# Kernel tuning notes

Measured on AMD Instinct MI355X. Metric: run time of the kernel, lower is better.

The kernel has to match this reference:

```python
import jax, jax.numpy as jnp
import numpy as np

N, E, D, H, ED = 50000, 600000, 128, 2, 5
C = D // H  # per-head channels = 64


def _lin(k, fan_in, fan_out):
    return jax.random.normal(k, (fan_out, fan_in), jnp.float32) / np.sqrt(fan_in)


def setup_inputs() -> dict:
    key = jax.random.key(0)
    ks = jax.random.split(key, 12)
    return {
        "x": jax.random.normal(ks[0], (N, D), jnp.float32),
        "edge_index": jax.random.randint(ks[1], (2, E), 0, N, dtype=jnp.int32),
        "edge_attr": jax.random.normal(ks[2], (E, ED), jnp.float32),
        "Wq": _lin(ks[3], D, D), "bq": jnp.zeros((D,), jnp.float32),
        "Wk": _lin(ks[4], D, D), "bk": jnp.zeros((D,), jnp.float32),
        "Wv": _lin(ks[5], D, D), "bv": jnp.zeros((D,), jnp.float32),
        "We": _lin(ks[6], ED, D),                       # lin_edge, bias=False in PyG
        "Wskip": _lin(ks[7], D, D), "bskip": jnp.zeros((D,), jnp.float32),
        "Wbeta": _lin(ks[8], 3 * D, 1),                 # lin_beta, bias=False
        "Wproj": _lin(ks[9], D, D), "bproj": jnp.zeros((D,), jnp.float32),
    }


def reference(x, edge_index, edge_attr, Wq, bq, Wk, bk, Wv, bv, We,
              Wskip, bskip, Wbeta, Wproj, bproj):
    src, dst = edge_index[0], edge_index[1]
    # node projections -> [N, H, C]
    q = (x @ Wq.T + bq).reshape(N, H, C)
    k = (x @ Wk.T + bk).reshape(N, H, C)
    v = (x @ Wv.T + bv).reshape(N, H, C)
    e = (edge_attr @ We.T).reshape(E, H, C)
    # gather per-edge, fold in edge features
    kj = k[src] + e                                   # [E, H, C]
    vj = v[src] + e                                   # [E, H, C]
    alpha = (q[dst] * kj).sum(-1) / np.sqrt(C)        # [E, H]
    # segment softmax over edges grouped by dst node
    amax = jax.ops.segment_max(alpha, dst, num_segments=N)   # [N, H]
    ex = jnp.exp(alpha - amax[dst])
    denom = jax.ops.segment_sum(ex, dst, num_segments=N)     # [N, H]
    w = ex / denom[dst]                               # [E, H]
    # scatter-aggregate weighted values, concat heads
    out = jax.ops.segment_sum(vj * w[:, :, None], dst, num_segments=N).reshape(N, D)
    # beta-gated skip connection
    x_r = x @ Wskip.T + bskip
    beta = jax.nn.sigmoid(jnp.concatenate([out, x_r, out - x_r], axis=-1) @ Wbeta.T)  # [N,1]
    out = beta * x_r + (1.0 - beta) * out
    # outer projection (dropout is identity in eval)
    return out @ Wproj.T + bproj
```

## Files before the change

kernel.cpp:

```cpp
#include <hip/hip_runtime.h>
#include <stdint.h>
#include <math.h>

#define D 128
#define EDIM 5

typedef __attribute__((ext_vector_type(8))) short bf16x8;
typedef __attribute__((ext_vector_type(4))) float f32x4;

__device__ __forceinline__ ushort f2b(float f) {
  union { float f; uint u; } v; v.f = f;
  uint u = v.u;
  return (ushort)((u + 0x7fff + ((u >> 16) & 1)) >> 16);
}
__device__ __forceinline__ float blo(uint u) {
  union { uint u; float f; } v; v.u = u << 16; return v.f;
}
__device__ __forceinline__ float bhi(uint u) {
  union { uint u; float f; } v; v.u = u & 0xffff0000u; return v.f;
}


__global__ void zero_int_kernel(int* __restrict__ p, int n) {
  int i = blockIdx.x * blockDim.x + threadIdx.x;
  if (i < n) p[i] = 0;
}

__global__ void hist_kernel(const int* __restrict__ ei, int* __restrict__ deg, int E) {
  int e = blockIdx.x * blockDim.x + threadIdx.x;
  if (e < E) atomicAdd(&deg[ei[(size_t)E + e]], 1);
}

__global__ __launch_bounds__(256) void scan_p1(const int* __restrict__ deg,
                                               int* __restrict__ off,
                                               int* __restrict__ blockSum, int n4) {
  __shared__ int waveTot[4];
  int idx = blockIdx.x * 256 + threadIdx.x;
  int4 v = make_int4(0, 0, 0, 0);
  if (idx < n4) v = ((const int4*)deg)[idx];
  int c0 = v.x, c1 = c0 + v.y, c2 = c1 + v.z, c3 = c2 + v.w;
  int tot = c3;
  int lane = threadIdx.x & 63, w = threadIdx.x >> 6;
  int incl = tot;
#pragma unroll
  for (int ofs = 1; ofs < 64; ofs <<= 1) {
    int t = __shfl_up(incl, ofs, 64);
    if (lane >= ofs) incl += t;
  }
  if (lane == 63) waveTot[w] = incl;
  __syncthreads();
  int wbase = 0;
  for (int i = 0; i < w; ++i) wbase += waveTot[i];
  int excl = wbase + incl - tot;
  if (idx < n4) {
    int4 o;
    o.x = excl; o.y = excl + c0; o.z = excl + c1; o.w = excl + c2;
    ((int4*)off)[idx] = o;
  }
  if (threadIdx.x == 255) blockSum[blockIdx.x] = wbase + incl;
}

__global__ void scan_p2(const int* __restrict__ blockSum, int* __restrict__ blockBase,
                        int* __restrict__ off_last, int nb) {
  int lane = threadIdx.x;
  int v = (lane < nb) ? blockSum[lane] : 0;
  int incl = v;
#pragma unroll
  for (int ofs = 1; ofs < 64; ofs <<= 1) {
    int t = __shfl_up(incl, ofs, 64);
    if (lane >= ofs) incl += t;
  }
  if (lane < nb) blockBase[lane] = incl - v;
  if (lane == 63) *off_last = incl;
}

__global__ __launch_bounds__(256) void scan_p3(int* __restrict__ off,
                                               const int* __restrict__ blockBase, int n4) {
  int idx = blockIdx.x * 256 + threadIdx.x;
  if (idx >= n4) return;
  int b = blockBase[blockIdx.x];
  int4 v = ((int4*)off)[idx];
  v.x += b; v.y += b; v.z += b; v.w += b;
  ((int4*)off)[idx] = v;
}

__global__ void scatter_kernel(const int* __restrict__ ei, const float* __restrict__ ea,
                               const int* __restrict__ off, int* __restrict__ cursor,
                               int* __restrict__ ssrc, uint4* __restrict__ easrt, int E) {
  int e = blockIdx.x * blockDim.x + threadIdx.x;
  if (e >= E) return;
  int dst = ei[(size_t)E + e];
  int pos = off[dst] + atomicAdd(&cursor[dst], 1);
  ssrc[pos] = ei[e];
  const float* p = ea + (size_t)e * EDIM;
  uint e0 = f2b(p[0]), e1 = f2b(p[1]), e2 = f2b(p[2]), e3 = f2b(p[3]), e4 = f2b(p[4]);
  easrt[pos] = make_uint4(e0 | (e1 << 16), e2 | (e3 << 16), e4, 0);
}


__global__ void cvt_x_kernel(const float* __restrict__ x, ushort* __restrict__ xb, int n4) {
  int i = blockIdx.x * blockDim.x + threadIdx.x;
  if (i >= n4) return;
  float4 v = ((const float4*)x)[i];
  ushort4 o;
  o.x = f2b(v.x); o.y = f2b(v.y); o.z = f2b(v.z); o.w = f2b(v.w);
  ((ushort4*)xb)[i] = o;
}

__global__ void cvt_w_kernel(const float* __restrict__ Wq, const float* __restrict__ Wk,
                             const float* __restrict__ Wv, const float* __restrict__ Wr,
                             const float* __restrict__ bq, const float* __restrict__ bk,
                             const float* __restrict__ bv, const float* __restrict__ br,
                             const float* __restrict__ Wp,
                             ushort* __restrict__ Wcat, float* __restrict__ bcat,
                             ushort* __restrict__ Wpb) {
  int i = blockIdx.x * blockDim.x + threadIdx.x;
  if (i < 512 * D) {
    int r = i >> 7;
    float v;
    if (r < 128)      v = Wq[i] * 0.125f;
    else if (r < 256) v = Wk[i - 128 * D];
    else if (r < 384) v = Wv[i - 256 * D];
    else              v = Wr[i - 384 * D];
    Wcat[i] = f2b(v);
  }
  if (i < D * D) Wpb[i] = f2b(Wp[i]);
  if (i < 512) {
    float v = (i < 128) ? bq[i] * 0.125f
            : (i < 256) ? bk[i - 128]
            : (i < 384) ? bv[i - 256] : br[i - 384];
    bcat[i] = v;
  }
}

template <int MODE>
__global__ __launch_bounds__(256) void gemm_kernel(
    const ushort* __restrict__ A, const ushort* __restrict__ B,
    const float* __restrict__ bias,
    float* __restrict__ q, ushort* __restrict__ kv, float* __restrict__ xr,
    float* __restrict__ out, int M)
{
  __shared__ __attribute__((aligned(16))) ushort As[128][128];
  __shared__ __attribute__((aligned(16))) ushort Bs[128][128];
  const int tid = threadIdx.x;
  const int rowBase = blockIdx.x * 128;
  const int colBase = blockIdx.y * 128;

#pragma unroll
  for (int it = 0; it < 8; ++it) {
    int i = it * 256 + tid;
    int r = i >> 4, c = i & 15;
    int sw = (c ^ (r & 7)) * 8;
    int gr = rowBase + r;
    uint4 av = make_uint4(0, 0, 0, 0);
    if (gr < M) av = *(const uint4*)(A + (size_t)gr * D + c * 8);
    *(uint4*)(&As[r][sw]) = av;
    uint4 bv4 = *(const uint4*)(B + (size_t)(colBase + r) * D + c * 8);
    *(uint4*)(&Bs[r][sw]) = bv4;
  }
  __syncthreads();

  const int lane = tid & 63;
  const int wave = tid >> 6;
  const int wm = (wave >> 1) * 64;
  const int wn = (wave & 1) * 64;
  const int lrow = lane & 15;
  const int kgrp = lane >> 4;

  f32x4 acc[4][4] = {};
#pragma unroll
  for (int ks = 0; ks < 4; ++ks) {
    int chunk = ks * 4 + kgrp;
    bf16x8 a[4], b[4];
#pragma unroll
    for (int m = 0; m < 4; ++m) {
      int r = wm + m * 16 + lrow;
      a[m] = *(const bf16x8*)&As[r][(chunk ^ (r & 7)) * 8];
    }
#pragma unroll
    for (int n = 0; n < 4; ++n) {
      int r = wn + n * 16 + lrow;
      b[n] = *(const bf16x8*)&Bs[r][(chunk ^ (r & 7)) * 8];
    }
#pragma unroll
    for (int m = 0; m < 4; ++m)
#pragma unroll
      for (int n = 0; n < 4; ++n)
        acc[m][n] = __builtin_amdgcn_mfma_f32_16x16x32_bf16(a[m], b[n], acc[m][n], 0, 0, 0);
  }

  const int orow = (lane >> 4) * 4;
  const int ocol = lane & 15;
#pragma unroll
  for (int m = 0; m < 4; ++m) {
#pragma unroll
    for (int n = 0; n < 4; ++n) {
      int col = colBase + wn + n * 16 + ocol;
      float bi = bias[col];
#pragma unroll
      for (int i = 0; i < 4; ++i) {
        int gr = rowBase + wm + m * 16 + orow + i;
        if (gr >= M) continue;
        float v = acc[m][n][i] + bi;
        if (MODE == 0) {
          int sel = col >> 7, c = col & 127;
          if (sel == 0)      q[(size_t)gr * D + c] = v;
          else if (sel == 1) kv[(size_t)gr * 2 * D + c] = f2b(v);
          else if (sel == 2) kv[(size_t)gr * 2 * D + D + c] = f2b(v);
          else               xr[(size_t)gr * D + c] = v;
        } else {
          out[(size_t)gr * D + col] = v;
        }
      }
    }
  }
}

__global__ __launch_bounds__(256) void node_attn_kernel(
    const float* __restrict__ q, const ushort* __restrict__ kv,
    const float* __restrict__ xr, ushort* __restrict__ g,
    const uint4* __restrict__ easrt, const float* __restrict__ We,
    const float* __restrict__ Wb,
    const int* __restrict__ off, const int* __restrict__ ssrc, int N)
{
  const int wid = threadIdx.x >> 6;
  const int lane = threadIdx.x & 63;
  const int node = blockIdx.x * 4 + wid;
  if (node >= N) return;
  const int grp = lane >> 4;
  const int i = lane & 15;
  const int di = i * 8;

  float qr[8];
  {
    float4 a = *(const float4*)(q + (size_t)node * D + di);
    float4 b = *(const float4*)(q + (size_t)node * D + di + 4);
    qr[0] = a.x; qr[1] = a.y; qr[2] = a.z; qr[3] = a.w;
    qr[4] = b.x; qr[5] = b.y; qr[6] = b.z; qr[7] = b.w;
  }

  float qwe[5];
  {
    const float* wp = We + (size_t)di * EDIM;
    float4 w[10];
#pragma unroll
    for (int t = 0; t < 10; ++t) w[t] = *(const float4*)(wp + 4 * t);
#pragma unroll
    for (int j = 0; j < 5; ++j) {
      float s = 0.f;
#pragma unroll
      for (int r = 0; r < 8; ++r) {
        int idx = r * 5 + j;
        s += qr[r] * ((const float*)&w[idx >> 2])[idx & 3];
      }
      qwe[j] = s;
    }
#pragma unroll
    for (int ofs = 1; ofs < 8; ofs <<= 1)
#pragma unroll
      for (int j = 0; j < 5; ++j) qwe[j] += __shfl_xor(qwe[j], ofs, 64);
  }

  const int beg = off[node], end = off[node + 1];
  float m = -INFINITY, s = 0.f;
  float o[8] = {0.f, 0.f, 0.f, 0.f, 0.f, 0.f, 0.f, 0.f};
  float wea[5] = {0.f, 0.f, 0.f, 0.f, 0.f};

  for (int pb = beg; pb < end; pb += 4) {
    int p = pb + grp;
    bool valid = p < end;
    int pl = valid ? p : beg;
    int src = ssrc[pl];
    uint4 eau = easrt[pl];
    float ea0 = blo(eau.x), ea1 = bhi(eau.x);
    float ea2 = blo(eau.y), ea3 = bhi(eau.y);
    float ea4 = blo(eau.z);

    const ushort* kp = kv + (size_t)src * 2 * D;
    uint4 ku = *(const uint4*)(kp + di);
    uint4 vu = *(const uint4*)(kp + D + di);

    float part = qr[0] * blo(ku.x) + qr[1] * bhi(ku.x)
               + qr[2] * blo(ku.y) + qr[3] * bhi(ku.y)
               + qr[4] * blo(ku.z) + qr[5] * bhi(ku.z)
               + qr[6] * blo(ku.w) + qr[7] * bhi(ku.w);
#pragma unroll
    for (int ofs = 1; ofs < 8; ofs <<= 1) part += __shfl_xor(part, ofs, 64);
    float eadot = qwe[0] * ea0 + qwe[1] * ea1 + qwe[2] * ea2 + qwe[3] * ea3 + qwe[4] * ea4;
    float alpha = valid ? (part + eadot) : -INFINITY;

    float nm = fmaxf(m, alpha);
    float scale = (m > -1e30f) ? __expf(m - nm) : 0.f;
    float pw = (alpha > -1e30f) ? __expf(alpha - nm) : 0.f;
    m = nm;
    s = s * scale + pw;
    o[0] = o[0] * scale + pw * blo(vu.x);
    o[1] = o[1] * scale + pw * bhi(vu.x);
    o[2] = o[2] * scale + pw * blo(vu.y);
    o[3] = o[3] * scale + pw * bhi(vu.y);
    o[4] = o[4] * scale + pw * blo(vu.z);
    o[5] = o[5] * scale + pw * bhi(vu.z);
    o[6] = o[6] * scale + pw * blo(vu.w);
    o[7] = o[7] * scale + pw * bhi(vu.w);
    wea[0] = wea[0] * scale + pw * ea0;
    wea[1] = wea[1] * scale + pw * ea1;
    wea[2] = wea[2] * scale + pw * ea2;
    wea[3] = wea[3] * scale + pw * ea3;
    wea[4] = wea[4] * scale + pw * ea4;
  }

#pragma unroll
  for (int ofs = 16; ofs < 64; ofs <<= 1) {
    float m2 = __shfl_xor(m, ofs, 64);
    float s2 = __shfl_xor(s, ofs, 64);
    float o2[8], w2[5];
#pragma unroll
    for (int j = 0; j < 8; ++j) o2[j] = __shfl_xor(o[j], ofs, 64);
#pragma unroll
    for (int j = 0; j < 5; ++j) w2[j] = __shfl_xor(wea[j], ofs, 64);
    float nm = fmaxf(m, m2);
    float e1 = (m > -1e30f) ? __expf(m - nm) : 0.f;
    float e2 = (m2 > -1e30f) ? __expf(m2 - nm) : 0.f;
    s = s * e1 + s2 * e2;
#pragma unroll
    for (int j = 0; j < 8; ++j) o[j] = o[j] * e1 + o2[j] * e2;
#pragma unroll
    for (int j = 0; j < 5; ++j) wea[j] = wea[j] * e1 + w2[j] * e2;
    m = nm;
  }

  float inv = (s > 0.f) ? (1.f / s) : 0.f;
#pragma unroll
  for (int j = 0; j < 8; ++j) o[j] *= inv;
#pragma unroll
  for (int j = 0; j < 5; ++j) wea[j] *= inv;

  {
    const float* wp = We + (size_t)di * EDIM;
    float4 w[10];
#pragma unroll
    for (int t = 0; t < 10; ++t) w[t] = *(const float4*)(wp + 4 * t);
#pragma unroll
    for (int r = 0; r < 8; ++r)
#pragma unroll
      for (int j = 0; j < 5; ++j) {
        int idx = r * 5 + j;
        o[r] += wea[j] * ((const float*)&w[idx >> 2])[idx & 3];
      }
  }

  float xrv[8];
  {
    float4 a = *(const float4*)(xr + (size_t)node * D + di);
    float4 b = *(const float4*)(xr + (size_t)node * D + di + 4);
    xrv[0] = a.x; xrv[1] = a.y; xrv[2] = a.z; xrv[3] = a.w;
    xrv[4] = b.x; xrv[5] = b.y; xrv[6] = b.z; xrv[7] = b.w;
  }
  float part = 0.f;
#pragma unroll
  for (int r = 0; r < 8; ++r) {
    float w1 = Wb[di + r] + Wb[256 + di + r];
    float w2 = Wb[128 + di + r] - Wb[256 + di + r];
    part += o[r] * w1 + xrv[r] * w2;
  }
#pragma unroll
  for (int ofs = 1; ofs < 16; ofs <<= 1) part += __shfl_xor(part, ofs, 64);
  float beta = 1.f / (1.f + __expf(-part));

  if (grp == 0) {
    uint pk[4];
#pragma unroll
    for (int r = 0; r < 4; ++r) {
      float g0 = beta * xrv[2 * r] + (1.f - beta) * o[2 * r];
      float g1 = beta * xrv[2 * r + 1] + (1.f - beta) * o[2 * r + 1];
      pk[r] = (uint)f2b(g0) | ((uint)f2b(g1) << 16);
    }
    *(uint4*)(g + (size_t)node * D + di) = make_uint4(pk[0], pk[1], pk[2], pk[3]);
  }
}


extern "C" void kernel_launch(void* const* d_in, const int* in_sizes, int n_in,
                              void* d_out, int out_size, void* d_ws, size_t ws_size,
                              hipStream_t stream)
{
  const float* x  = (const float*)d_in[0];
  const int*   ei = (const int*)d_in[1];
  const float* ea = (const float*)d_in[2];
  const float* Wq = (const float*)d_in[3];
  const float* bq = (const float*)d_in[4];
  const float* Wk = (const float*)d_in[5];
  const float* bk = (const float*)d_in[6];
  const float* Wv = (const float*)d_in[7];
  const float* bv = (const float*)d_in[8];
  const float* We = (const float*)d_in[9];
  const float* Wr = (const float*)d_in[10];
  const float* br = (const float*)d_in[11];
  const float* Wb = (const float*)d_in[12];
  const float* Wp = (const float*)d_in[13];
  const float* bp = (const float*)d_in[14];

  const int N = in_sizes[0] / D;
  const int E = in_sizes[1] / 2;
  float* out = (float*)d_out;

  char* ws = (char*)d_ws;
  size_t o = 0;
  auto alloc = [&](size_t bytes) -> void* {
    void* p = ws + o;
    o = (o + bytes + 255) & ~(size_t)255;
    return p;
  };
  ushort* xb     = (ushort*)alloc((size_t)N * D * sizeof(ushort));
  float*  q      = (float*)alloc((size_t)N * D * sizeof(float));
  ushort* kv     = (ushort*)alloc((size_t)N * 2 * D * sizeof(ushort));
  float*  xr     = (float*)alloc((size_t)N * D * sizeof(float));
  ushort* g      = (ushort*)alloc((size_t)N * D * sizeof(ushort));
  ushort* Wcat   = (ushort*)alloc((size_t)512 * D * sizeof(ushort));
  float*  bcat   = (float*)alloc(512 * sizeof(float));
  ushort* Wpb    = (ushort*)alloc((size_t)D * D * sizeof(ushort));
  int*    deg    = (int*)alloc((size_t)N * sizeof(int));
  int*    cursor = (int*)alloc((size_t)N * sizeof(int));
  int*    offs   = (int*)alloc((size_t)(N + 1) * sizeof(int));
  int*    ssrc   = (int*)alloc((size_t)E * sizeof(int));
  uint4*  easrt  = (uint4*)alloc((size_t)E * sizeof(uint4));
  int*    bsum   = (int*)alloc(64 * sizeof(int));
  int*    bbase  = (int*)alloc(64 * sizeof(int));

  const int n4 = N / 4;
  const int nb = (n4 + 255) / 256;

  zero_int_kernel<<<(N + 255) / 256, 256, 0, stream>>>(deg, N);
  zero_int_kernel<<<(N + 255) / 256, 256, 0, stream>>>(cursor, N);
  hist_kernel<<<(E + 255) / 256, 256, 0, stream>>>(ei, deg, E);
  scan_p1<<<nb, 256, 0, stream>>>(deg, offs, bsum, n4);
  scan_p2<<<1, 64, 0, stream>>>(bsum, bbase, offs + N, nb);
  scan_p3<<<nb, 256, 0, stream>>>(offs, bbase, n4);
  scatter_kernel<<<(E + 255) / 256, 256, 0, stream>>>(ei, ea, offs, cursor, ssrc, easrt, E);

  cvt_x_kernel<<<(N * D / 4 + 255) / 256, 256, 0, stream>>>(x, xb, N * D / 4);
  cvt_w_kernel<<<(512 * D + 255) / 256, 256, 0, stream>>>(Wq, Wk, Wv, Wr, bq, bk, bv, br,
                                                          Wp, Wcat, bcat, Wpb);

  dim3 g0((N + 127) / 128, 4);
  gemm_kernel<0><<<g0, 256, 0, stream>>>(xb, Wcat, bcat, q, kv, xr, nullptr, N);

  node_attn_kernel<<<(N + 3) / 4, 256, 0, stream>>>(q, kv, xr, g, easrt, We, Wb,
                                                    offs, ssrc, N);

  dim3 g1((N + 127) / 128, 1);
  gemm_kernel<1><<<g1, 256, 0, stream>>>(g, Wpb, bp, nullptr, nullptr, nullptr, out, N);
}
```

Before: 256.0 us.

## Fuse x conversion into projection GEMM, precompute q·We, lazy softmax rescale

Removes the separate x-to-bf16 and cursor-zeroing kernels by folding them into the projection GEMM and scan kernels. Adds a folded Wq·We block to the weight matrix so the GEMM also emits per-node q·We terms, replacing the per-node shuffle reduction in the attention kernel. Stores q and x_r as bf16 instead of fp32 to cut memory traffic, and uses 64-row GEMM tiles that loop over all five column blocks. The attention loop now prefetches the next edge's gather and skips the online-softmax rescale unless the running max grows by more than a threshold. These trade some precision and a larger GEMM per block for fewer launches and less traffic.

Result: faster. 241.2 us (-5.8%).

```diff
diff --git a/kernel.cpp b/kernel.cpp
--- a/kernel.cpp
+++ b/kernel.cpp
@@ -75,13 +75,15 @@
 }
 
 __global__ __launch_bounds__(256) void scan_p3(int* __restrict__ off,
-                                               const int* __restrict__ blockBase, int n4) {
+                                               const int* __restrict__ blockBase,
+                                               int* __restrict__ cursor, int n4) {
   int idx = blockIdx.x * 256 + threadIdx.x;
   if (idx >= n4) return;
   int b = blockBase[blockIdx.x];
   int4 v = ((int4*)off)[idx];
   v.x += b; v.y += b; v.z += b; v.w += b;
   ((int4*)off)[idx] = v;
+  ((int4*)cursor)[idx] = make_int4(0, 0, 0, 0);
 }
 
 __global__ void scatter_kernel(const int* __restrict__ ei, const float* __restrict__ ea,
@@ -97,21 +99,11 @@
   easrt[pos] = make_uint4(e0 | (e1 << 16), e2 | (e3 << 16), e4, 0);
 }
 
-
-__global__ void cvt_x_kernel(const float* __restrict__ x, ushort* __restrict__ xb, int n4) {
-  int i = blockIdx.x * blockDim.x + threadIdx.x;
-  if (i >= n4) return;
-  float4 v = ((const float4*)x)[i];
-  ushort4 o;
-  o.x = f2b(v.x); o.y = f2b(v.y); o.z = f2b(v.z); o.w = f2b(v.w);
-  ((ushort4*)xb)[i] = o;
-}
-
 __global__ void cvt_w_kernel(const float* __restrict__ Wq, const float* __restrict__ Wk,
                              const float* __restrict__ Wv, const float* __restrict__ Wr,
                              const float* __restrict__ bq, const float* __restrict__ bk,
                              const float* __restrict__ bv, const float* __restrict__ br,
-                             const float* __restrict__ Wp,
+                             const float* __restrict__ We, const float* __restrict__ Wp,
                              ushort* __restrict__ Wcat, float* __restrict__ bcat,
                              ushort* __restrict__ Wpb) {
   int i = blockIdx.x * blockDim.x + threadIdx.x;
@@ -123,6 +115,18 @@
     else if (r < 384) v = Wv[i - 256 * D];
     else              v = Wr[i - 384 * D];
     Wcat[i] = f2b(v);
+  } else if (i < 512 * D + 128 * D) {
+    int ie = i - 512 * D;
+    int r = ie >> 7, c = ie & 127;
+    int h = r >> 3, j = r & 7;
+    float v = 0.f;
+    if (h < 2 && j < 5) {
+      for (int d = 0; d < 64; ++d) {
+        int dd = h * 64 + d;
+        v += We[(size_t)dd * EDIM + j] * 0.125f * Wq[(size_t)dd * D + c];
+      }
+    }
+    Wcat[(size_t)(512 + r) * D + c] = f2b(v);
   }
   if (i < D * D) Wpb[i] = f2b(Wp[i]);
   if (i < 512) {
@@ -130,50 +134,155 @@
             : (i < 256) ? bk[i - 128]
             : (i < 384) ? bv[i - 256] : br[i - 384];
     bcat[i] = v;
-  }
-}
-
-template <int MODE>
-__global__ __launch_bounds__(256) void gemm_kernel(
-    const ushort* __restrict__ A, const ushort* __restrict__ B,
-    const float* __restrict__ bias,
-    float* __restrict__ q, ushort* __restrict__ kv, float* __restrict__ xr,
-    float* __restrict__ out, int M)
+  } else if (i < 640) {
+    int t = i - 512;
+    int h = t >> 3, j = t & 7;
+    float v = 0.f;
+    if (h < 2 && j < 5) {
+      for (int d = 0; d < 64; ++d) {
+        int dd = h * 64 + d;
+        v += bq[dd] * 0.125f * We[(size_t)dd * EDIM + j];
+      }
+    }
+    bcat[i] = v;
+  }
+}
+
+__global__ __launch_bounds__(256) void proj_gemm_kernel(
+    const float* __restrict__ x, const ushort* __restrict__ Wcat,
+    const float* __restrict__ bcat,
+    ushort* __restrict__ q, ushort* __restrict__ kv, ushort* __restrict__ xr,
+    float* __restrict__ qwe, int M)
 {
-  __shared__ __attribute__((aligned(16))) ushort As[128][128];
+  __shared__ __attribute__((aligned(16))) ushort As[64][128];
   __shared__ __attribute__((aligned(16))) ushort Bs[128][128];
   const int tid = threadIdx.x;
-  const int rowBase = blockIdx.x * 128;
-  const int colBase = blockIdx.y * 128;
-
+  const int rowBase = blockIdx.x * 64;
+
+#pragma unroll
+  for (int it = 0; it < 4; ++it) {
+    int i = it * 256 + tid;
+    int r = i >> 4, c = i & 15;
+    int gr = rowBase + r;
+    float4 a0 = make_float4(0.f, 0.f, 0.f, 0.f), a1 = a0;
+    if (gr < M) {
+      a0 = *(const float4*)(x + (size_t)gr * D + c * 8);
+      a1 = *(const float4*)(x + (size_t)gr * D + c * 8 + 4);
+    }
+    uint4 w;
+    w.x = (uint)f2b(a0.x) | ((uint)f2b(a0.y) << 16);
+    w.y = (uint)f2b(a0.z) | ((uint)f2b(a0.w) << 16);
+    w.z = (uint)f2b(a1.x) | ((uint)f2b(a1.y) << 16);
+    w.w = (uint)f2b(a1.z) | ((uint)f2b(a1.w) << 16);
+    *(uint4*)(&As[r][(c ^ (r & 7)) * 8]) = w;
+  }
+
+  const int lane = tid & 63;
+  const int wave = tid >> 6;
+  const int wm = (wave >> 1) * 32;
+  const int wn = (wave & 1) * 64;
+  const int lrow = lane & 15;
+  const int kgrp = lane >> 4;
+  const int orow = (lane >> 4) * 4;
+  const int ocol = lane & 15;
+
+  for (int cb = 0; cb < 5; ++cb) {
+#pragma unroll
+    for (int it = 0; it < 8; ++it) {
+      int i = it * 256 + tid;
+      int r = i >> 4, c = i & 15;
+      uint4 bv4 = *(const uint4*)(Wcat + (size_t)(cb * 128 + r) * D + c * 8);
+      *(uint4*)(&Bs[r][(c ^ (r & 7)) * 8]) = bv4;
+    }
+    __syncthreads();
+
+    f32x4 acc[2][4] = {};
+#pragma unroll
+    for (int ks = 0; ks < 4; ++ks) {
+      int chunk = ks * 4 + kgrp;
+      bf16x8 a[2], b[4];
+#pragma unroll
+      for (int m = 0; m < 2; ++m) {
+        int r = wm + m * 16 + lrow;
+        a[m] = *(const bf16x8*)&As[r][(chunk ^ (r & 7)) * 8];
+      }
+#pragma unroll
+      for (int n = 0; n < 4; ++n) {
+        int r = wn + n * 16 + lrow;
+        b[n] = *(const bf16x8*)&Bs[r][(chunk ^ (r & 7)) * 8];
+      }
+#pragma unroll
+      for (int m = 0; m < 2; ++m)
+#pragma unroll
+        for (int n = 0; n < 4; ++n)
+          acc[m][n] = __builtin_amdgcn_mfma_f32_16x16x32_bf16(a[m], b[n], acc[m][n], 0, 0, 0);
+    }
+
+#pragma unroll
+    for (int m = 0; m < 2; ++m) {
+#pragma unroll
+      for (int n = 0; n < 4; ++n) {
+        int col = cb * 128 + wn + n * 16 + ocol;
+        float bi = bcat[col];
+        int sel = col >> 7, c = col & 127;
+#pragma unroll
+        for (int ii = 0; ii < 4; ++ii) {
+          int gr = rowBase + wm + m * 16 + orow + ii;
+          if (gr >= M) continue;
+          float v = acc[m][n][ii] + bi;
+          if (sel == 0)      q[(size_t)gr * D + c] = f2b(v);
+          else if (sel == 1) kv[(size_t)gr * 2 * D + c] = f2b(v);
+          else if (sel == 2) kv[(size_t)gr * 2 * D + D + c] = f2b(v);
+          else if (sel == 3) xr[(size_t)gr * D + c] = f2b(v);
+          else if (c < 16)   qwe[(size_t)gr * 16 + c] = v;
+        }
+      }
+    }
+    __syncthreads();
+  }
+}
+
+__global__ __launch_bounds__(256) void out_gemm_kernel(
+    const ushort* __restrict__ g, const ushort* __restrict__ Wpb,
+    const float* __restrict__ bp, float* __restrict__ out, int M)
+{
+  __shared__ __attribute__((aligned(16))) ushort As[64][128];
+  __shared__ __attribute__((aligned(16))) ushort Bs[128][128];
+  const int tid = threadIdx.x;
+  const int rowBase = blockIdx.x * 64;
+
+#pragma unroll
+  for (int it = 0; it < 4; ++it) {
+    int i = it * 256 + tid;
+    int r = i >> 4, c = i & 15;
+    int gr = rowBase + r;
+    uint4 av = make_uint4(0, 0, 0, 0);
+    if (gr < M) av = *(const uint4*)(g + (size_t)gr * D + c * 8);
+    *(uint4*)(&As[r][(c ^ (r & 7)) * 8]) = av;
+  }
 #pragma unroll
   for (int it = 0; it < 8; ++it) {
     int i = it * 256 + tid;
     int r = i >> 4, c = i & 15;
-    int sw = (c ^ (r & 7)) * 8;
-    int gr = rowBase + r;
-    uint4 av = make_uint4(0, 0, 0, 0);
-    if (gr < M) av = *(const uint4*)(A + (size_t)gr * D + c * 8);
-    *(uint4*)(&As[r][sw]) = av;
-    uint4 bv4 = *(const uint4*)(B + (size_t)(colBase + r) * D + c * 8);
-    *(uint4*)(&Bs[r][sw]) = bv4;
+    uint4 bv4 = *(const uint4*)(Wpb + (size_t)r * D + c * 8);
+    *(uint4*)(&Bs[r][(c ^ (r & 7)) * 8]) = bv4;
   }
   __syncthreads();
 
   const int lane = tid & 63;
   const int wave = tid >> 6;
-  const int wm = (wave >> 1) * 64;
+  const int wm = (wave >> 1) * 32;
   const int wn = (wave & 1) * 64;
   const int lrow = lane & 15;
   const int kgrp = lane >> 4;
 
-  f32x4 acc[4][4] = {};
+  f32x4 acc[2][4] = {};
 #pragma unroll
   for (int ks = 0; ks < 4; ++ks) {
     int chunk = ks * 4 + kgrp;
-    bf16x8 a[4], b[4];
-#pragma unroll
-    for (int m = 0; m < 4; ++m) {
+    bf16x8 a[2], b[4];
+#pragma unroll
+    for (int m = 0; m < 2; ++m) {
       int r = wm + m * 16 + lrow;
       a[m] = *(const bf16x8*)&As[r][(chunk ^ (r & 7)) * 8];
     }
@@ -183,7 +292,7 @@
       b[n] = *(const bf16x8*)&Bs[r][(chunk ^ (r & 7)) * 8];
     }
 #pragma unroll
-    for (int m = 0; m < 4; ++m)
+    for (int m = 0; m < 2; ++m)
 #pragma unroll
       for (int n = 0; n < 4; ++n)
         acc[m][n] = __builtin_amdgcn_mfma_f32_16x16x32_bf16(a[m], b[n], acc[m][n], 0, 0, 0);
@@ -192,35 +301,26 @@
   const int orow = (lane >> 4) * 4;
   const int ocol = lane & 15;
 #pragma unroll
-  for (int m = 0; m < 4; ++m) {
+  for (int m = 0; m < 2; ++m) {
 #pragma unroll
     for (int n = 0; n < 4; ++n) {
-      int col = colBase + wn + n * 16 + ocol;
-      float bi = bias[col];
-#pragma unroll
-      for (int i = 0; i < 4; ++i) {
-        int gr = rowBase + wm + m * 16 + orow + i;
+      int col = wn + n * 16 + ocol;
+      float bi = bp[col];
+#pragma unroll
+      for (int ii = 0; ii < 4; ++ii) {
+        int gr = rowBase + wm + m * 16 + orow + ii;
         if (gr >= M) continue;
-        float v = acc[m][n][i] + bi;
-        if (MODE == 0) {
-          int sel = col >> 7, c = col & 127;
-          if (sel == 0)      q[(size_t)gr * D + c] = v;
-          else if (sel == 1) kv[(size_t)gr * 2 * D + c] = f2b(v);
-          else if (sel == 2) kv[(size_t)gr * 2 * D + D + c] = f2b(v);
-          else               xr[(size_t)gr * D + c] = v;
-        } else {
-          out[(size_t)gr * D + col] = v;
-        }
+        out[(size_t)gr * D + col] = acc[m][n][ii] + bi;
       }
     }
   }
 }
 
 __global__ __launch_bounds__(256) void node_attn_kernel(
-    const float* __restrict__ q, const ushort* __restrict__ kv,
-    const float* __restrict__ xr, ushort* __restrict__ g,
-    const uint4* __restrict__ easrt, const float* __restrict__ We,
-    const float* __restrict__ Wb,
+    const ushort* __restrict__ q, const ushort* __restrict__ kv,
+    const ushort* __restrict__ xr, ushort* __restrict__ g,
+    const float* __restrict__ qwe, const uint4* __restrict__ easrt,
+    const float* __restrict__ We, const float* __restrict__ Wb,
     const int* __restrict__ off, const int* __restrict__ ssrc, int N)
 {
   const int wid = threadIdx.x >> 6;
@@ -230,35 +330,19 @@
   const int grp = lane >> 4;
   const int i = lane & 15;
   const int di = i * 8;
+  const int head = i >> 3;
 
   float qr[8];
   {
-    float4 a = *(const float4*)(q + (size_t)node * D + di);
-    float4 b = *(const float4*)(q + (size_t)node * D + di + 4);
-    qr[0] = a.x; qr[1] = a.y; qr[2] = a.z; qr[3] = a.w;
-    qr[4] = b.x; qr[5] = b.y; qr[6] = b.z; qr[7] = b.w;
-  }
-
-  float qwe[5];
+    uint4 qa = *(const uint4*)(q + (size_t)node * D + di);
+    qr[0] = blo(qa.x); qr[1] = bhi(qa.x); qr[2] = blo(qa.y); qr[3] = bhi(qa.y);
+    qr[4] = blo(qa.z); qr[5] = bhi(qa.z); qr[6] = blo(qa.w); qr[7] = bhi(qa.w);
+  }
+  float qw[5];
   {
-    const float* wp = We + (size_t)di * EDIM;
-    float4 w[10];
-#pragma unroll
-    for (int t = 0; t < 10; ++t) w[t] = *(const float4*)(wp + 4 * t);
-#pragma unroll
-    for (int j = 0; j < 5; ++j) {
-      float s = 0.f;
-#pragma unroll
-      for (int r = 0; r < 8; ++r) {
-        int idx = r * 5 + j;
-        s += qr[r] * ((const float*)&w[idx >> 2])[idx & 3];
-      }
-      qwe[j] = s;
-    }
-#pragma unroll
-    for (int ofs = 1; ofs < 8; ofs <<= 1)
-#pragma unroll
-      for (int j = 0; j < 5; ++j) qwe[j] += __shfl_xor(qwe[j], ofs, 64);
+    const float* qp = qwe + (size_t)node * 16 + head * 8;
+    float4 t = *(const float4*)qp;
+    qw[0] = t.x; qw[1] = t.y; qw[2] = t.z; qw[3] = t.w; qw[4] = qp[4];
   }
 
   const int beg = off[node], end = off[node + 1];
@@ -266,47 +350,65 @@
   float o[8] = {0.f, 0.f, 0.f, 0.f, 0.f, 0.f, 0.f, 0.f};
   float wea[5] = {0.f, 0.f, 0.f, 0.f, 0.f};
 
-  for (int pb = beg; pb < end; pb += 4) {
-    int p = pb + grp;
-    bool valid = p < end;
-    int pl = valid ? p : beg;
-    int src = ssrc[pl];
-    uint4 eau = easrt[pl];
-    float ea0 = blo(eau.x), ea1 = bhi(eau.x);
-    float ea2 = blo(eau.y), ea3 = bhi(eau.y);
-    float ea4 = blo(eau.z);
-
-    const ushort* kp = kv + (size_t)src * 2 * D;
-    uint4 ku = *(const uint4*)(kp + di);
-    uint4 vu = *(const uint4*)(kp + D + di);
-
-    float part = qr[0] * blo(ku.x) + qr[1] * bhi(ku.x)
-               + qr[2] * blo(ku.y) + qr[3] * bhi(ku.y)
-               + qr[4] * blo(ku.z) + qr[5] * bhi(ku.z)
-               + qr[6] * blo(ku.w) + qr[7] * bhi(ku.w);
-#pragma unroll
-    for (int ofs = 1; ofs < 8; ofs <<= 1) part += __shfl_xor(part, ofs, 64);
-    float eadot = qwe[0] * ea0 + qwe[1] * ea1 + qwe[2] * ea2 + qwe[3] * ea3 + qwe[4] * ea4;
-    float alpha = valid ? (part + eadot) : -INFINITY;
-
-    float nm = fmaxf(m, alpha);
-    float scale = (m > -1e30f) ? __expf(m - nm) : 0.f;
-    float pw = (alpha > -1e30f) ? __expf(alpha - nm) : 0.f;
-    m = nm;
-    s = s * scale + pw;
-    o[0] = o[0] * scale + pw * blo(vu.x);
-    o[1] = o[1] * scale + pw * bhi(vu.x);
-    o[2] = o[2] * scale + pw * blo(vu.y);
-    o[3] = o[3] * scale + pw * bhi(vu.y);
-    o[4] = o[4] * scale + pw * blo(vu.z);
-    o[5] = o[5] * scale + pw * bhi(vu.z);
-    o[6] = o[6] * scale + pw * blo(vu.w);
-    o[7] = o[7] * scale + pw * bhi(vu.w);
-    wea[0] = wea[0] * scale + pw * ea0;
-    wea[1] = wea[1] * scale + pw * ea1;
-    wea[2] = wea[2] * scale + pw * ea2;
-    wea[3] = wea[3] * scale + pw * ea3;
-    wea[4] = wea[4] * scale + pw * ea4;
+  if (beg < end) {
+    int p0 = beg + grp;
+    bool valid_c = p0 < end;
+    int pl = valid_c ? p0 : beg;
+    int src_c = ssrc[pl];
+    uint4 eau_c = easrt[pl];
+    const ushort* kp0 = kv + (size_t)src_c * (2 * D);
+    uint4 ku_c = *(const uint4*)(kp0 + di);
+    uint4 vu_c = *(const uint4*)(kp0 + D + di);
+
+    for (int pb = beg; pb < end; pb += 4) {
+      int pn = pb + 4 + grp;
+      bool valid_n = pn < end;
+      int pln = valid_n ? pn : pl;
+      int src_n = ssrc[pln];
+      uint4 eau_n = easrt[pln];
+
+      float ea0 = blo(eau_c.x), ea1 = bhi(eau_c.x), ea2 = blo(eau_c.y),
+            ea3 = bhi(eau_c.y), ea4 = blo(eau_c.z);
+      float part = qr[0] * blo(ku_c.x) + qr[1] * bhi(ku_c.x)
+                 + qr[2] * blo(ku_c.y) + qr[3] * bhi(ku_c.y)
+                 + qr[4] * blo(ku_c.z) + qr[5] * bhi(ku_c.z)
+                 + qr[6] * blo(ku_c.w) + qr[7] * bhi(ku_c.w);
+#pragma unroll
+      for (int ofs = 1; ofs < 8; ofs <<= 1) part += __shfl_xor(part, ofs, 64);
+      float eadot = qw[0] * ea0 + qw[1] * ea1 + qw[2] * ea2 + qw[3] * ea3 + qw[4] * ea4;
+      float alpha = valid_c ? (part + eadot) : -INFINITY;
+
+      const ushort* kpn = kv + (size_t)src_n * (2 * D);
+      uint4 ku_n = *(const uint4*)(kpn + di);
+      uint4 vu_n = *(const uint4*)(kpn + D + di);
+
+      float v0 = blo(vu_c.x), v1 = bhi(vu_c.x), v2 = blo(vu_c.y), v3 = bhi(vu_c.y),
+            v4 = blo(vu_c.z), v5 = bhi(vu_c.z), v6 = blo(vu_c.w), v7 = bhi(vu_c.w);
+
+      if (__any(alpha > m + 8.f)) {
+        float nm = fmaxf(m, alpha);
+        float scale = (m > -1e30f) ? __expf(m - nm) : 0.f;
+        float pw = (alpha > -1e30f) ? __expf(alpha - nm) : 0.f;
+        m = nm;
+        s = s * scale + pw;
+        o[0] = o[0] * scale + pw * v0; o[1] = o[1] * scale + pw * v1;
+        o[2] = o[2] * scale + pw * v2; o[3] = o[3] * scale + pw * v3;
+        o[4] = o[4] * scale + pw * v4; o[5] = o[5] * scale + pw * v5;
+        o[6] = o[6] * scale + pw * v6; o[7] = o[7] * scale + pw * v7;
+        wea[0] = wea[0] * scale + pw * ea0; wea[1] = wea[1] * scale + pw * ea1;
+        wea[2] = wea[2] * scale + pw * ea2; wea[3] = wea[3] * scale + pw * ea3;
+        wea[4] = wea[4] * scale + pw * ea4;
+      } else {
+        float pw = (alpha > -1e30f) ? __expf(alpha - m) : 0.f;
+        s += pw;
+        o[0] += pw * v0; o[1] += pw * v1; o[2] += pw * v2; o[3] += pw * v3;
+        o[4] += pw * v4; o[5] += pw * v5; o[6] += pw * v6; o[7] += pw * v7;
+        wea[0] += pw * ea0; wea[1] += pw * ea1; wea[2] += pw * ea2;
+        wea[3] += pw * ea3; wea[4] += pw * ea4;
+      }
+
+      ku_c = ku_n; vu_c = vu_n; eau_c = eau_n; valid_c = valid_n; pl = pln;
+    }
   }
 
 #pragma unroll
@@ -351,10 +453,9 @@
 
   float xrv[8];
   {
-    float4 a = *(const float4*)(xr + (size_t)node * D + di);
-    float4 b = *(const float4*)(xr + (size_t)node * D + di + 4);
-    xrv[0] = a.x; xrv[1] = a.y; xrv[2] = a.z; xrv[3] = a.w;
-    xrv[4] = b.x; xrv[5] = b.y; xrv[6] = b.z; xrv[7] = b.w;
+    uint4 xa = *(const uint4*)(xr + (size_t)node * D + di);
+    xrv[0] = blo(xa.x); xrv[1] = bhi(xa.x); xrv[2] = blo(xa.y); xrv[3] = bhi(xa.y);
+    xrv[4] = blo(xa.z); xrv[5] = bhi(xa.z); xrv[6] = blo(xa.w); xrv[7] = bhi(xa.w);
   }
   float part = 0.f;
 #pragma unroll
@@ -411,13 +512,13 @@
     o = (o + bytes + 255) & ~(size_t)255;
     return p;
   };
-  ushort* xb     = (ushort*)alloc((size_t)N * D * sizeof(ushort));
-  float*  q      = (float*)alloc((size_t)N * D * sizeof(float));
+  ushort* q      = (ushort*)alloc((size_t)N * D * sizeof(ushort));
   ushort* kv     = (ushort*)alloc((size_t)N * 2 * D * sizeof(ushort));
-  float*  xr     = (float*)alloc((size_t)N * D * sizeof(float));
+  ushort* xr     = (ushort*)alloc((size_t)N * D * sizeof(ushort));
   ushort* g      = (ushort*)alloc((size_t)N * D * sizeof(ushort));
-  ushort* Wcat   = (ushort*)alloc((size_t)512 * D * sizeof(ushort));
-  float*  bcat   = (float*)alloc(512 * sizeof(float));
+  float*  qwe    = (float*)alloc((size_t)N * 16 * sizeof(float));
+  ushort* Wcat   = (ushort*)alloc((size_t)640 * D * sizeof(ushort));
+  float*  bcat   = (float*)alloc(640 * sizeof(float));
   ushort* Wpb    = (ushort*)alloc((size_t)D * D * sizeof(ushort));
   int*    deg    = (int*)alloc((size_t)N * sizeof(int));
   int*    cursor = (int*)alloc((size_t)N * sizeof(int));
@@ -431,23 +532,19 @@
   const int nb = (n4 + 255) / 256;
 
   zero_int_kernel<<<(N + 255) / 256, 256, 0, stream>>>(deg, N);
-  zero_int_kernel<<<(N + 255) / 256, 256, 0, stream>>>(cursor, N);
   hist_kernel<<<(E + 255) / 256, 256, 0, stream>>>(ei, deg, E);
   scan_p1<<<nb, 256, 0, stream>>>(deg, offs, bsum, n4);
   scan_p2<<<1, 64, 0, stream>>>(bsum, bbase, offs + N, nb);
-  scan_p3<<<nb, 256, 0, stream>>>(offs, bbase, n4);
+  scan_p3<<<nb, 256, 0, stream>>>(offs, bbase, cursor, n4);
   scatter_kernel<<<(E + 255) / 256, 256, 0, stream>>>(ei, ea, offs, cursor, ssrc, easrt, E);
 
-  cvt_x_kernel<<<(N * D / 4 + 255) / 256, 256, 0, stream>>>(x, xb, N * D / 4);
-  cvt_w_kernel<<<(512 * D + 255) / 256, 256, 0, stream>>>(Wq, Wk, Wv, Wr, bq, bk, bv, br,
-                                                          Wp, Wcat, bcat, Wpb);
-
-  dim3 g0((N + 127) / 128, 4);
-  gemm_kernel<0><<<g0, 256, 0, stream>>>(xb, Wcat, bcat, q, kv, xr, nullptr, N);
-
-  node_attn_kernel<<<(N + 3) / 4, 256, 0, stream>>>(q, kv, xr, g, easrt, We, Wb,
+  cvt_w_kernel<<<(512 * D + 128 * D + 255) / 256, 256, 0, stream>>>(
+      Wq, Wk, Wv, Wr, bq, bk, bv, br, We, Wp, Wcat, bcat, Wpb);
+
+  proj_gemm_kernel<<<(N + 63) / 64, 256, 0, stream>>>(x, Wcat, bcat, q, kv, xr, qwe, N);
+
+  node_attn_kernel<<<(N + 3) / 4, 256, 0, stream>>>(q, kv, xr, g, qwe, easrt, We, Wb,
                                                     offs, ssrc, N);
 
-  dim3 g1((N + 127) / 128, 1);
-  gemm_kernel<1><<<g1, 256, 0, stream>>>(g, Wpb, bp, nullptr, nullptr, nullptr, out, N);
-}
+  out_gemm_kernel<<<(N + 63) / 64, 256, 0, stream>>>(g, Wpb, bp, out, N);
+}
```
